# Optimization experiments

Hardware: AMD Instinct MI355X
Metric: run time of the kernel (lower is better)

The kernel has to match this reference:

```python
import jax, jax.numpy as jnp
import numpy as np

B, L, NE, DOUT = 4, 4096, 64, 64
DI = 128          # backbone model dim (hardcoded d_inner in MambaDoc)
NL = 2            # num_layers
H = 2             # num_heads
N = 128           # state_dim
G = 1             # num_groups
CONV = 4          # conv_size
DIN = 2 * DI      # expand=2 -> 256 inner channels of the mixer
P = DIN // H      # headdim = 128
CCH = DIN + 2 * G * N      # 512 conv channels (x, B, C)
DPROJ = 2 * DIN + 2 * G * N + H  # 770 in_proj output width


def setup_inputs() -> dict:
    key = jax.random.key(0)
    ks = jax.random.split(key, 8)
    s = lambda k, shape, sc: (jax.random.normal(k, shape, jnp.float32) * sc)
    return {
        "x": s(ks[0], (B, L, NE), 1.0),
        "in_w": s(ks[1], (DI, NE), (1.0 / NE) ** 0.5),
        "in_b": jnp.zeros((DI,), jnp.float32),
        "out_w": s(ks[2], (DOUT, DI), (1.0 / DI) ** 0.5),
        "out_b": jnp.zeros((DOUT,), jnp.float32),
        "l_rms_w": jnp.ones((NL, DI), jnp.float32),
        "l_in_w": s(ks[3], (NL, DPROJ, DI), (1.0 / DI) ** 0.5),
        "conv_w": s(ks[4], (NL, CCH, CONV), (1.0 / CONV) ** 0.5),
        "conv_b": jnp.zeros((NL, CCH), jnp.float32),
        "dt_bias": s(ks[5], (NL, H), 0.1),
        "A_log": jnp.zeros((NL, H), jnp.float32),   # A = -exp(A_log) = -1
        "D_p": jnp.ones((NL, H), jnp.float32),
        "gnorm_w": jnp.ones((NL, DIN), jnp.float32),
        "l_out_w": s(ks[6], (NL, DI, DIN), (1.0 / DIN) ** 0.5),
        "fnorm_w": jnp.ones((DI,), jnp.float32),
    }


def _rms(x, w, eps=1e-5):
    return x * jax.lax.rsqrt(jnp.mean(x * x, -1, keepdims=True) + eps) * w


def _mamba_layer(x, rms_w, in_w, cw, cb, dtb, a_log, d, gnw, ow):
    # x: (B,L,DI)
    h = _rms(x, rms_w)
    zxbcdt = jnp.einsum("bld,ed->ble", h, in_w)  # (B,L,770)
    z, xBC, dt = jnp.split(zxbcdt, [DIN, DIN + CCH], axis=-1)
    # causal depthwise conv over time, conv_size taps
    xp = jnp.pad(xBC, ((0, 0), (CONV - 1, 0), (0, 0)))
    xc = cb + sum(xp[:, k:k + L, :] * cw[:, k] for k in range(CONV))
    xc = jax.nn.silu(xc)
    xs, Bm, Cm = jnp.split(xc, [DIN, DIN + G * N], axis=-1)
    xs = xs.reshape(B, L, H, P)
    dt = jax.nn.softplus(dt + dtb)                 # (B,L,H)
    dA = jnp.exp(dt * (-jnp.exp(a_log)))           # (B,L,H) discrete decay

    def step(hc, inp):
        dA_t, dt_t, x_t, B_t, C_t = inp  # (B,H),(B,H),(B,H,P),(B,N),(B,N)
        hc = hc * dA_t[:, :, None, None] + (dt_t[:, :, None] * x_t)[..., None] * B_t[:, None, None, :]
        y = jnp.einsum("bhpn,bn->bhp", hc, C_t)
        return hc, y

    h0 = jnp.zeros((B, H, P, N), x.dtype)
    seq = (jnp.moveaxis(dA, 1, 0), jnp.moveaxis(dt, 1, 0), jnp.moveaxis(xs, 1, 0),
           jnp.moveaxis(Bm, 1, 0), jnp.moveaxis(Cm, 1, 0))
    _, ys = jax.lax.scan(step, h0, seq)
    y = jnp.moveaxis(ys, 0, 1)                     # (B,L,H,P)
    y = y + xs * d[None, None, :, None]            # D skip connection
    y = _rms(y.reshape(B, L, DIN) * jax.nn.silu(z), gnw)  # gated RMSNorm
    return x + jnp.einsum("ble,de->bld", y, ow)


def reference(x, in_w, in_b, out_w, out_b, l_rms_w, l_in_w, conv_w, conv_b,
              dt_bias, A_log, D_p, gnorm_w, l_out_w, fnorm_w):
    xp = jnp.einsum("bln,dn->bld", x, in_w) + in_b
    h = xp
    for i in range(NL):
        h = _mamba_layer(h, l_rms_w[i], l_in_w[i], conv_w[i], conv_b[i],
                         dt_bias[i], A_log[i], D_p[i], gnorm_w[i], l_out_w[i])
    h = _rms(h, fnorm_w)            # backbone final norm
    out = xp + h                    # outer residual in MambaDoc.forward
    return jnp.einsum("bld,od->blo", out, out_w) + out_b
```

## Files before the change

### kernel.cpp

```cpp
#include <hip/hip_runtime.h>
#include <cstddef>
#include <cstdint>


#define LSEQ 4096
#define MTOK 16384

typedef unsigned short u16;
typedef _Float16 f16x8 __attribute__((ext_vector_type(8)));
typedef float f32x4 __attribute__((ext_vector_type(4)));

__device__ __forceinline__ u16 f2h(float x) {
    return __builtin_bit_cast(u16, (_Float16)x);
}
__device__ __forceinline__ float h2f(u16 u) {
    return (float)__builtin_bit_cast(_Float16, u);
}
__device__ __forceinline__ float silu_f(float x) { return x / (1.f + __expf(-x)); }

__device__ __forceinline__ void async_lds16(const void* g, void* l) {
    __builtin_amdgcn_global_load_lds(
        (const __attribute__((address_space(1))) unsigned int*)g,
        (__attribute__((address_space(3))) unsigned int*)l, 16, 0, 0);
}

__device__ __forceinline__ uint4 cvt8(const float* __restrict__ src) {
    float4 a = *(const float4*)src;
    float4 b = *(const float4*)(src + 4);
    union { u16 u[8]; uint4 q; } pk;
    pk.u[0] = f2h(a.x); pk.u[1] = f2h(a.y); pk.u[2] = f2h(a.z); pk.u[3] = f2h(a.w);
    pk.u[4] = f2h(b.x); pk.u[5] = f2h(b.y); pk.u[6] = f2h(b.z); pk.u[7] = f2h(b.w);
    return pk.q;
}

__device__ __forceinline__ uint4 cvt8g(const float* __restrict__ src,
                                       const float* __restrict__ gw) {
    float4 a = *(const float4*)src;
    float4 b = *(const float4*)(src + 4);
    float4 ga = *(const float4*)gw;
    float4 gb = *(const float4*)(gw + 4);
    union { u16 u[8]; uint4 q; } pk;
    pk.u[0] = f2h(a.x * ga.x); pk.u[1] = f2h(a.y * ga.y);
    pk.u[2] = f2h(a.z * ga.z); pk.u[3] = f2h(a.w * ga.w);
    pk.u[4] = f2h(b.x * gb.x); pk.u[5] = f2h(b.y * gb.y);
    pk.u[6] = f2h(b.z * gb.z); pk.u[7] = f2h(b.w * gb.w);
    return pk.q;
}

__global__ __launch_bounds__(256) void gemm_rms0_kernel(
    const float* __restrict__ xf, const float* __restrict__ wf,
    const float* __restrict__ bias, const float* __restrict__ rmsw,
    u16* __restrict__ xp16, u16* __restrict__ hbuf16, u16* __restrict__ hn16)
{
    __shared__ u16 sA[64 * 64];
    __shared__ u16 sW[128 * 64];
    __shared__ float red[64][33];
    __shared__ float srstd[64];
    const int m0 = blockIdx.y * 64;
    const int tid = threadIdx.x, wid = tid >> 6, lane = tid & 63;
    const int wm = (wid >> 1) * 32, wn = (wid & 1) * 64;
    const int quad = lane >> 4, cl = lane & 15;
    #pragma unroll
    for (int i = 0; i < 2; i++) {
        int ck = i * 256 + tid;
        int r = ck >> 3, cc = ck & 7;
        int csw = (cc ^ (r & 7)) << 3;
        *(uint4*)&sA[ck * 8] = cvt8(xf + (size_t)(m0 + r) * 64 + csw);
    }
    #pragma unroll
    for (int i = 0; i < 4; i++) {
        int ck = i * 256 + tid;
        int r = ck >> 3, cc = ck & 7;
        int csw = (cc ^ (r & 7)) << 3;
        *(uint4*)&sW[ck * 8] = cvt8(wf + (size_t)r * 64 + csw);
    }
    __syncthreads();
    f32x4 acc[2][4];
    #pragma unroll
    for (int i = 0; i < 2; i++)
        #pragma unroll
        for (int j = 0; j < 4; j++) acc[i][j] = f32x4{0.f, 0.f, 0.f, 0.f};
    #pragma unroll
    for (int ks = 0; ks < 2; ks++) {
        f16x8 af[2], wv[4];
        int kc = ks * 4 + quad;
        #pragma unroll
        for (int i = 0; i < 2; i++) {
            int r = wm + i * 16 + cl;
            af[i] = *(const f16x8*)&sA[r * 64 + ((kc ^ (r & 7)) << 3)];
        }
        #pragma unroll
        for (int j = 0; j < 4; j++) {
            int r = wn + j * 16 + cl;
            wv[j] = *(const f16x8*)&sW[r * 64 + ((kc ^ (r & 7)) << 3)];
        }
        #pragma unroll
        for (int i = 0; i < 2; i++)
            #pragma unroll
            for (int j = 0; j < 4; j++)
                acc[i][j] = __builtin_amdgcn_mfma_f32_16x16x32_f16(
                    af[i], wv[j], acc[i][j], 0, 0, 0);
    }
    const int slot = (wid & 1) * 16 + cl;
    #pragma unroll
    for (int i = 0; i < 2; i++)
        #pragma unroll
        for (int r = 0; r < 4; r++) {
            int t = wm + i * 16 + quad * 4 + r;
            float ssp = 0.f;
            #pragma unroll
            for (int j = 0; j < 4; j++) {
                int n = wn + j * 16 + cl;
                float v = acc[i][j][r] + bias[n];
                acc[i][j][r] = v;
                ssp += v * v;
            }
            red[t][slot] = ssp;
        }
    __syncthreads();
    if (tid < 64) {
        float s = 0.f;
        #pragma unroll
        for (int sl = 0; sl < 32; sl++) s += red[tid][sl];
        srstd[tid] = rsqrtf(s * (1.f / 128.f) + 1e-5f);
    }
    __syncthreads();
    #pragma unroll
    for (int i = 0; i < 2; i++)
        #pragma unroll
        for (int r = 0; r < 4; r++) {
            int t = wm + i * 16 + quad * 4 + r;
            size_t ob = (size_t)(m0 + t) * 128;
            float rstd = srstd[t];
            #pragma unroll
            for (int j = 0; j < 4; j++) {
                int n = wn + j * 16 + cl;
                float v = acc[i][j][r];
                u16 vh = f2h(v);
                xp16[ob + n] = vh;
                hbuf16[ob + n] = vh;
                hn16[ob + n] = f2h(v * rstd * rmsw[n]);
            }
        }
}

__global__ __launch_bounds__(256) void gemm_inproj_kernel(
    const u16* __restrict__ A, const float* __restrict__ Wf,
    u16* __restrict__ zx16, float* __restrict__ dtb, float* __restrict__ Sb,
    const float* __restrict__ dt_bias, const float* __restrict__ A_log)
{
    __shared__ u16 sA[128 * 64];
    __shared__ u16 sW[128 * 64];
    __shared__ float sdt[2][128];
    const int K = 128, N = 770;
    const int n0 = blockIdx.x * 128, m0 = blockIdx.y * 128;
    const int tid = threadIdx.x, wid = tid >> 6, lane = tid & 63;
    const int wm = (wid >> 1) * 64, wn = (wid & 1) * 64;
    const int quad = lane >> 4, cl = lane & 15;
    f32x4 acc[4][4];
    #pragma unroll
    for (int i = 0; i < 4; i++)
        #pragma unroll
        for (int j = 0; j < 4; j++) acc[i][j] = f32x4{0.f, 0.f, 0.f, 0.f};

    for (int k0 = 0; k0 < K; k0 += 64) {
        #pragma unroll
        for (int i = 0; i < 4; i++) {
            int ck = i * 256 + tid;
            int r = ck >> 3, cc = ck & 7;
            int csw = (cc ^ (r & 7)) << 3;
            async_lds16(A + (size_t)(m0 + r) * K + k0 + csw,
                        (void*)(sA + (i * 256 + (tid & ~63)) * 8));
        }
        #pragma unroll
        for (int i = 0; i < 4; i++) {
            int ck = i * 256 + tid;
            int r = ck >> 3, cc = ck & 7;
            int csw = (cc ^ (r & 7)) << 3;
            int rr = n0 + r; if (rr >= N) rr = N - 1;
            *(uint4*)&sW[ck * 8] = cvt8(Wf + (size_t)rr * K + k0 + csw);
        }
        __syncthreads();
        #pragma unroll
        for (int ks = 0; ks < 2; ks++) {
            f16x8 af[4], wv[4];
            int kc = ks * 4 + quad;
            #pragma unroll
            for (int i = 0; i < 4; i++) {
                int r = wm + i * 16 + cl;
                af[i] = *(const f16x8*)&sA[r * 64 + ((kc ^ (r & 7)) << 3)];
            }
            #pragma unroll
            for (int j = 0; j < 4; j++) {
                int r = wn + j * 16 + cl;
                wv[j] = *(const f16x8*)&sW[r * 64 + ((kc ^ (r & 7)) << 3)];
            }
            #pragma unroll
            for (int i = 0; i < 4; i++)
                #pragma unroll
                for (int j = 0; j < 4; j++)
                    acc[i][j] = __builtin_amdgcn_mfma_f32_16x16x32_f16(
                        af[i], wv[j], acc[i][j], 0, 0, 0);
        }
        __syncthreads();
    }
    if (blockIdx.x < 6) {
        #pragma unroll
        for (int i = 0; i < 4; i++) {
            int m = m0 + wm + i * 16 + quad * 4;
            #pragma unroll
            for (int j = 0; j < 4; j++) {
                int n = n0 + wn + j * 16 + cl;
                #pragma unroll
                for (int r = 0; r < 4; r++)
                    zx16[(size_t)(m + r) * 768 + n] = f2h(acc[i][j][r]);
            }
        }
    } else {
        if ((wid & 1) == 0 && cl < 2) {
            #pragma unroll
            for (int i = 0; i < 4; i++)
                #pragma unroll
                for (int r = 0; r < 4; r++)
                    sdt[cl][wm + i * 16 + quad * 4 + r] = acc[i][0][r];
        }
        __syncthreads();
        const int hh = tid >> 7, t = tid & 127;
        float raw = sdt[hh][t] + dt_bias[hh];
        float dt = fmaxf(raw, 0.f) + log1pf(__expf(-fabsf(raw)));
        dtb[(size_t)(m0 + t) * 2 + hh] = dt;
        float ad = -__expf(A_log[hh]) * dt;
        __syncthreads();
        sdt[hh][t] = ad;
        __syncthreads();
        for (int off = 1; off < 128; off <<= 1) {
            float add = (t >= off) ? sdt[hh][t - off] : 0.f;
            __syncthreads();
            sdt[hh][t] += add;
            __syncthreads();
        }
        Sb[(size_t)(m0 + t) * 2 + hh] = sdt[hh][t];
    }
}

__global__ __launch_bounds__(512) void chunkstate_conv_kernel(
    const u16* __restrict__ zx16, const float* __restrict__ cw,
    const float* __restrict__ cb, const float* __restrict__ dtb,
    const float* __restrict__ Sb, u16* __restrict__ Hb)
{
    __shared__ u16 raw[2560 * 8];
    __shared__ u16 XT[128 * 128];
    __shared__ u16 BT[128 * 128];
    __shared__ float scw[2][128][4];
    __shared__ float scb[2][128];
    __shared__ float ssw[128];
    const int c = blockIdx.x, h = blockIdx.y, b = blockIdx.z;
    const int tid = threadIdx.x, wid = tid >> 6, lane = tid & 63;
    const int quad = lane >> 4, cl = lane & 15;
    const int tok0 = b * LSEQ + c * 128;
    for (int idx = tid; idx < 256; idx += 512) {
        int grp = idx >> 7, j = idx & 127;
        int ch = grp ? (256 + j) : (128 * h + j);
        float4 w4 = *(const float4*)&cw[ch * 4];
        scw[grp][j][0] = w4.x; scw[grp][j][1] = w4.y;
        scw[grp][j][2] = w4.z; scw[grp][j][3] = w4.w;
        scb[grp][j] = cb[ch];
    }
    if (tid < 128) {
        float Sl = Sb[(size_t)(tok0 + 127) * 2 + h];
        ssw[tid] = __expf(Sl - Sb[(size_t)(tok0 + tid) * 2 + h])
                   * dtb[(size_t)(tok0 + tid) * 2 + h];
    }
    #pragma unroll
    for (int i = 0; i < 5; i++) {
        int ck = i * 512 + tid;
        int r = ck >> 4; if (r > 130) r = 130;
        int cc = ck & 15;
        int tok = tok0 - 3 + r; if (tok < 0) tok = 0;
        async_lds16(zx16 + (size_t)tok * 768 + 256 + 128 * h + ((cc ^ (r & 15)) << 3),
                    (void*)(raw + (i * 512 + (tid & ~63)) * 8));
    }
    __syncthreads();
    if (c == 0 && tid < 48) *(uint4*)&raw[tid * 8] = make_uint4(0, 0, 0, 0);
    __syncthreads();
    #pragma unroll
    for (int it = 0; it < 4; it++) {
        int idx = it * 512 + tid;
        int s = idx & 127, pg = idx >> 7;
        f16x8 v[4];
        #pragma unroll
        for (int k = 0; k < 4; k++) {
            int rr = s + k;
            v[k] = *(const f16x8*)&raw[rr * 128 + ((pg ^ (rr & 15)) << 3)];
        }
        #pragma unroll
        for (int j = 0; j < 8; j++) {
            int p = pg * 8 + j;
            float o = scb[0][p] + (float)v[0][j] * scw[0][p][0]
                    + (float)v[1][j] * scw[0][p][1]
                    + (float)v[2][j] * scw[0][p][2]
                    + (float)v[3][j] * scw[0][p][3];
            o = silu_f(o);
            XT[p * 128 + (((s >> 3) ^ (p & 15)) << 3) + (s & 7)] = f2h(o);
        }
    }
    __syncthreads();
    #pragma unroll
    for (int i = 0; i < 5; i++) {
        int ck = i * 512 + tid;
        int r = ck >> 4; if (r > 130) r = 130;
        int cc = ck & 15;
        int tok = tok0 - 3 + r; if (tok < 0) tok = 0;
        async_lds16(zx16 + (size_t)tok * 768 + 512 + ((cc ^ (r & 15)) << 3),
                    (void*)(raw + (i * 512 + (tid & ~63)) * 8));
    }
    __syncthreads();
    if (c == 0 && tid < 48) *(uint4*)&raw[tid * 8] = make_uint4(0, 0, 0, 0);
    __syncthreads();
    #pragma unroll
    for (int it = 0; it < 4; it++) {
        int idx = it * 512 + tid;
        int s = idx & 127, ng = idx >> 7;
        f16x8 v[4];
        #pragma unroll
        for (int k = 0; k < 4; k++) {
            int rr = s + k;
            v[k] = *(const f16x8*)&raw[rr * 128 + ((ng ^ (rr & 15)) << 3)];
        }
        float wsv = ssw[s];
        #pragma unroll
        for (int j = 0; j < 8; j++) {
            int n = ng * 8 + j;
            float o = scb[1][n] + (float)v[0][j] * scw[1][n][0]
                    + (float)v[1][j] * scw[1][n][1]
                    + (float)v[2][j] * scw[1][n][2]
                    + (float)v[3][j] * scw[1][n][3];
            o = silu_f(o) * wsv;
            BT[n * 128 + (((s >> 3) ^ (n & 15)) << 3) + (s & 7)] = f2h(o);
        }
    }
    __syncthreads();
    const size_t blk = ((size_t)((b * 2 + h) * 32 + c)) << 14;
    const int wm = (wid >> 1) * 32, wn = (wid & 1) * 64;
    f32x4 acc[2][4];
    #pragma unroll
    for (int i = 0; i < 2; i++)
        #pragma unroll
        for (int j = 0; j < 4; j++) acc[i][j] = f32x4{0.f, 0.f, 0.f, 0.f};
    #pragma unroll
    for (int ks = 0; ks < 4; ks++) {
        f16x8 xa[2], bb[4];
        int kc = ks * 4 + quad;
        #pragma unroll
        for (int i = 0; i < 2; i++) {
            int r = wm + i * 16 + cl;
            xa[i] = *(const f16x8*)&XT[r * 128 + ((kc ^ (r & 15)) << 3)];
        }
        #pragma unroll
        for (int j = 0; j < 4; j++) {
            int r = wn + j * 16 + cl;
            bb[j] = *(const f16x8*)&BT[r * 128 + ((kc ^ (r & 15)) << 3)];
        }
        #pragma unroll
        for (int i = 0; i < 2; i++)
            #pragma unroll
            for (int j = 0; j < 4; j++)
                acc[i][j] = __builtin_amdgcn_mfma_f32_16x16x32_f16(
                    xa[i], bb[j], acc[i][j], 0, 0, 0);
    }
    u16* out = Hb + blk;
    #pragma unroll
    for (int i = 0; i < 2; i++)
        #pragma unroll
        for (int j = 0; j < 4; j++)
            #pragma unroll
            for (int r = 0; r < 4; r++)
                out[(size_t)(wm + i * 16 + quad * 4 + r) * 128 + wn + j * 16 + cl]
                    = f2h(acc[i][j][r]);
}

__global__ __launch_bounds__(256) void statecombine_kernel(
    const float* __restrict__ Sb, const u16* __restrict__ Hb,
    u16* __restrict__ Hbf)
{
    __shared__ float sdec[32];
    const int h = blockIdx.y, b = blockIdx.z;
    const int e2 = blockIdx.x * 256 + threadIdx.x;
    if (threadIdx.x < 32)
        sdec[threadIdx.x] =
            __expf(Sb[(size_t)(b * LSEQ + threadIdx.x * 128 + 127) * 2 + h]);
    const size_t base2 = ((size_t)((b * 2 + h) * 32)) << 13;
    const unsigned int* src = (const unsigned int*)Hb;
    unsigned int* dst = (unsigned int*)Hbf;
    unsigned int v[32];
    #pragma unroll
    for (int c = 0; c < 32; c++)
        v[c] = src[base2 + ((size_t)c << 13) + e2];
    __syncthreads();
    float s0 = 0.f, s1 = 0.f;
    #pragma unroll
    for (int c = 0; c < 32; c++) {
        union { u16 u[2]; unsigned int q; } pk;
        pk.u[0] = f2h(s0); pk.u[1] = f2h(s1);
        dst[base2 + ((size_t)c << 13) + e2] = pk.q;
        float d = sdec[c];
        s0 = d * s0 + h2f((u16)(v[c] & 0xffffu));
        s1 = d * s1 + h2f((u16)(v[c] >> 16));
    }
}

__global__ __launch_bounds__(512) void ssd_ph_kernel(
    const u16* __restrict__ zx16, const u16* __restrict__ Hbf,
    const float* __restrict__ dtb, const float* __restrict__ Sb,
    const float* __restrict__ cw, const float* __restrict__ cb,
    const float* __restrict__ Dp, u16* __restrict__ g16)
{
    __shared__ u16 raw[2560 * 8];
    __shared__ u16 XT[128 * 128];
    __shared__ u16 Btok[128 * 128];
    __shared__ u16 Ctok[128 * 128];
    __shared__ float sS[128], sdt[128];
    __shared__ float scw[3][128][4];
    __shared__ float scb[3][128];
    const int c = blockIdx.x, h = blockIdx.y, b = blockIdx.z;
    const int tid = threadIdx.x, wid = tid >> 6, lane = tid & 63;
    const int quad = lane >> 4, cl = lane & 15;
    const int tok0 = b * LSEQ + c * 128;
    const size_t blk = ((size_t)((b * 2 + h) * 32 + c)) << 14;
    for (int idx = tid; idx < 384; idx += 512) {
        int grp = idx >> 7, j = idx & 127;
        int ch = (grp == 0) ? (128 * h + j) : (grp == 1 ? 256 + j : 384 + j);
        float4 w4 = *(const float4*)&cw[ch * 4];
        scw[grp][j][0] = w4.x; scw[grp][j][1] = w4.y;
        scw[grp][j][2] = w4.z; scw[grp][j][3] = w4.w;
        scb[grp][j] = cb[ch];
    }
    if (tid < 128) {
        sS[tid] = Sb[(size_t)(tok0 + tid) * 2 + h];
        sdt[tid] = dtb[(size_t)(tok0 + tid) * 2 + h];
    }
    #pragma unroll
    for (int i = 0; i < 5; i++) {
        int ck = i * 512 + tid;
        int r = ck >> 4; if (r > 130) r = 130;
        int cc = ck & 15;
        int tok = tok0 - 3 + r; if (tok < 0) tok = 0;
        async_lds16(zx16 + (size_t)tok * 768 + 256 + 128 * h + ((cc ^ (r & 15)) << 3),
                    (void*)(raw + (i * 512 + (tid & ~63)) * 8));
    }
    __syncthreads();
    if (c == 0 && tid < 48) *(uint4*)&raw[tid * 8] = make_uint4(0, 0, 0, 0);
    __syncthreads();
    #pragma unroll
    for (int it = 0; it < 4; it++) {
        int idx = it * 512 + tid;
        int s = idx & 127, pg = idx >> 7;
        f16x8 v[4];
        #pragma unroll
        for (int k = 0; k < 4; k++) {
            int rr = s + k;
            v[k] = *(const f16x8*)&raw[rr * 128 + ((pg ^ (rr & 15)) << 3)];
        }
        #pragma unroll
        for (int j = 0; j < 8; j++) {
            int p = pg * 8 + j;
            float o = scb[0][p] + (float)v[0][j] * scw[0][p][0]
                    + (float)v[1][j] * scw[0][p][1]
                    + (float)v[2][j] * scw[0][p][2]
                    + (float)v[3][j] * scw[0][p][3];
            XT[p * 128 + (((s >> 3) ^ (p & 15)) << 3) + (s & 7)] = f2h(silu_f(o));
        }
    }
    __syncthreads();
    #pragma unroll
    for (int i = 0; i < 5; i++) {
        int ck = i * 512 + tid;
        int r = ck >> 4; if (r > 130) r = 130;
        int cc = ck & 15;
        int tok = tok0 - 3 + r; if (tok < 0) tok = 0;
        async_lds16(zx16 + (size_t)tok * 768 + 512 + ((cc ^ (r & 15)) << 3),
                    (void*)(raw + (i * 512 + (tid & ~63)) * 8));
    }
    __syncthreads();
    if (c == 0 && tid < 48) *(uint4*)&raw[tid * 8] = make_uint4(0, 0, 0, 0);
    __syncthreads();
    #pragma unroll
    for (int it = 0; it < 4; it++) {
        int idx = it * 512 + tid;
        int t = idx & 127, ng = idx >> 7;
        f16x8 v[4];
        #pragma unroll
        for (int k = 0; k < 4; k++) {
            int rr = t + k;
            v[k] = *(const f16x8*)&raw[rr * 128 + ((ng ^ (rr & 15)) << 3)];
        }
        union { u16 u[8]; uint4 q; } pk;
        #pragma unroll
        for (int j = 0; j < 8; j++) {
            int n = ng * 8 + j;
            float o = scb[1][n] + (float)v[0][j] * scw[1][n][0]
                    + (float)v[1][j] * scw[1][n][1]
                    + (float)v[2][j] * scw[1][n][2]
                    + (float)v[3][j] * scw[1][n][3];
            pk.u[j] = f2h(silu_f(o));
        }
        *(uint4*)&Btok[t * 128 + ((ng ^ (t & 15)) << 3)] = pk.q;
    }
    __syncthreads();
    #pragma unroll
    for (int i = 0; i < 5; i++) {
        int ck = i * 512 + tid;
        int r = ck >> 4; if (r > 130) r = 130;
        int cc = ck & 15;
        int tok = tok0 - 3 + r; if (tok < 0) tok = 0;
        async_lds16(zx16 + (size_t)tok * 768 + 640 + ((cc ^ (r & 15)) << 3),
                    (void*)(raw + (i * 512 + (tid & ~63)) * 8));
    }
    __syncthreads();
    if (c == 0 && tid < 48) *(uint4*)&raw[tid * 8] = make_uint4(0, 0, 0, 0);
    __syncthreads();
    #pragma unroll
    for (int it = 0; it < 4; it++) {
        int idx = it * 512 + tid;
        int t = idx & 127, ng = idx >> 7;
        f16x8 v[4];
        #pragma unroll
        for (int k = 0; k < 4; k++) {
            int rr = t + k;
            v[k] = *(const f16x8*)&raw[rr * 128 + ((ng ^ (rr & 15)) << 3)];
        }
        union { u16 u[8]; uint4 q; } pk;
        #pragma unroll
        for (int j = 0; j < 8; j++) {
            int n = ng * 8 + j;
            float o = scb[2][n] + (float)v[0][j] * scw[2][n][0]
                    + (float)v[1][j] * scw[2][n][1]
                    + (float)v[2][j] * scw[2][n][2]
                    + (float)v[3][j] * scw[2][n][3];
            pk.u[j] = f2h(silu_f(o));
        }
        *(uint4*)&Ctok[t * 128 + ((ng ^ (t & 15)) << 3)] = pk.q;
    }
    __syncthreads();
    #pragma unroll
    for (int i = 0; i < 4; i++) {
        int ck = i * 512 + tid;
        int r = ck >> 4, cc = ck & 15;
        async_lds16(Hbf + blk + (size_t)r * 128 + ((cc ^ (r & 15)) << 3),
                    (void*)(raw + (i * 512 + (tid & ~63)) * 8));
    }
    __syncthreads();
    const int wm = (wid >> 1) * 32, wn = (wid & 1) * 64;
    f32x4 acc[2][4];
    #pragma unroll
    for (int i = 0; i < 2; i++)
        #pragma unroll
        for (int j = 0; j < 4; j++) acc[i][j] = f32x4{0.f, 0.f, 0.f, 0.f};
    #pragma unroll
    for (int ks = 0; ks < 4; ks++) {
        f16x8 ca[2], hb[4];
        int kc = ks * 4 + quad;
        #pragma unroll
        for (int i = 0; i < 2; i++) {
            int r = wm + i * 16 + cl;
            ca[i] = *(const f16x8*)&Ctok[r * 128 + ((kc ^ (r & 15)) << 3)];
        }
        #pragma unroll
        for (int j = 0; j < 4; j++) {
            int r = wn + j * 16 + cl;
            hb[j] = *(const f16x8*)&raw[r * 128 + ((kc ^ (r & 15)) << 3)];
        }
        #pragma unroll
        for (int i = 0; i < 2; i++)
            #pragma unroll
            for (int j = 0; j < 4; j++)
                acc[i][j] = __builtin_amdgcn_mfma_f32_16x16x32_f16(
                    ca[i], hb[j], acc[i][j], 0, 0, 0);
    }
    #pragma unroll
    for (int i = 0; i < 2; i++)
        #pragma unroll
        for (int r = 0; r < 4; r++) {
            float e = __expf(sS[wm + i * 16 + quad * 4 + r]);
            #pragma unroll
            for (int j = 0; j < 4; j++) acc[i][j][r] *= e;
        }
    f32x4 sacc[2][4];
    #pragma unroll
    for (int i = 0; i < 2; i++)
        #pragma unroll
        for (int j = 0; j < 4; j++) sacc[i][j] = f32x4{0.f, 0.f, 0.f, 0.f};
    #pragma unroll
    for (int ks = 0; ks < 4; ks++) {
        f16x8 cs[2], bs[4];
        int kc = ks * 4 + quad;
        #pragma unroll
        for (int i2 = 0; i2 < 2; i2++) {
            int r = wm + i2 * 16 + cl;
            cs[i2] = *(const f16x8*)&Ctok[r * 128 + ((kc ^ (r & 15)) << 3)];
        }
        #pragma unroll
        for (int j = 0; j < 4; j++) {
            int r = wn + j * 16 + cl;
            bs[j] = *(const f16x8*)&Btok[r * 128 + ((kc ^ (r & 15)) << 3)];
        }
        #pragma unroll
        for (int i2 = 0; i2 < 2; i2++)
            #pragma unroll
            for (int j = 0; j < 4; j++)
                if (wm + i2 * 16 + 15 >= wn + j * 16)
                    sacc[i2][j] = __builtin_amdgcn_mfma_f32_16x16x32_f16(
                        cs[i2], bs[j], sacc[i2][j], 0, 0, 0);
    }
    __syncthreads();
    #pragma unroll
    for (int i2 = 0; i2 < 2; i2++)
        #pragma unroll
        for (int r = 0; r < 4; r++) {
            int t = wm + i2 * 16 + quad * 4 + r;
            float Stv = sS[t];
            #pragma unroll
            for (int j = 0; j < 4; j++) {
                int s = wn + j * 16 + cl;
                float gv = 0.f;
                if (s <= t) gv = sacc[i2][j][r] * __expf(Stv - sS[s]) * sdt[s];
                raw[t * 128 + (((s >> 3) ^ (t & 15)) << 3) + (s & 7)] = f2h(gv);
            }
        }
    __syncthreads();
    #pragma unroll
    for (int ks = 0; ks < 4; ks++) {
        f16x8 ga[2], xb[4];
        int kc = ks * 4 + quad;
        #pragma unroll
        for (int i = 0; i < 2; i++) {
            int r = wm + i * 16 + cl;
            ga[i] = *(const f16x8*)&raw[r * 128 + ((kc ^ (r & 15)) << 3)];
        }
        #pragma unroll
        for (int j = 0; j < 4; j++) {
            int r = wn + j * 16 + cl;
            xb[j] = *(const f16x8*)&XT[r * 128 + ((kc ^ (r & 15)) << 3)];
        }
        #pragma unroll
        for (int i = 0; i < 2; i++)
            #pragma unroll
            for (int j = 0; j < 4; j++)
                acc[i][j] = __builtin_amdgcn_mfma_f32_16x16x32_f16(
                    ga[i], xb[j], acc[i][j], 0, 0, 0);
    }
    const float dco = Dp[h];
    #pragma unroll
    for (int i = 0; i < 2; i++)
        #pragma unroll
        for (int r = 0; r < 4; r++) {
            int t = wm + i * 16 + quad * 4 + r;
            u16* row = g16 + (size_t)(tok0 + t) * 256 + h * 128;
            #pragma unroll
            for (int j = 0; j < 4; j++) {
                int p = wn + j * 16 + cl;
                float xv = h2f(XT[p * 128 + (((t >> 3) ^ (p & 15)) << 3) + (t & 7)]);
                float zv = h2f(zx16[(size_t)(tok0 + t) * 768 + h * 128 + p]);
                row[p] = f2h((acc[i][j][r] + dco * xv) * silu_f(zv));
            }
        }
}

__global__ __launch_bounds__(256) void gemm_outrms_kernel(
    const u16* __restrict__ A, const float* __restrict__ Wf,
    const float* __restrict__ gnw, const float* __restrict__ rmsw,
    u16* __restrict__ xp16, u16* __restrict__ hbuf16, u16* __restrict__ hn16,
    const float* __restrict__ out_wf, const float* __restrict__ out_b,
    float* __restrict__ dout, int mode)
{
    __shared__ u16 sA[64 * 64];
    __shared__ u16 sW[128 * 64];
    __shared__ float red[64][33];
    __shared__ float srstd[64];
    __shared__ float redp[64][5];
    __shared__ float rstdg[64];
    __shared__ u16 hn2[64 * 128];
    __shared__ u16 ow[64 * 128];
    const int K = 256;
    const int m0 = blockIdx.y * 64;
    const int tid = threadIdx.x, wid = tid >> 6, lane = tid & 63;
    const int wm = (wid >> 1) * 32, wn = (wid & 1) * 64;
    const int quad = lane >> 4, cl = lane & 15;
    {
        int t = tid >> 2, q = tid & 3;
        const u16* row = A + (size_t)(m0 + t) * 256 + q * 64;
        float ss = 0.f;
        #pragma unroll
        for (int u = 0; u < 8; u++) {
            f16x8 v = *(const f16x8*)&row[u * 8];
            #pragma unroll
            for (int j = 0; j < 8; j++) { float f = (float)v[j]; ss += f * f; }
        }
        redp[t][q] = ss;
    }
    __syncthreads();
    if (tid < 64)
        rstdg[tid] = rsqrtf((redp[tid][0] + redp[tid][1] + redp[tid][2]
                             + redp[tid][3]) * (1.f / 256.f) + 1e-5f);
    f32x4 acc[2][4];
    #pragma unroll
    for (int i = 0; i < 2; i++)
        #pragma unroll
        for (int j = 0; j < 4; j++) acc[i][j] = f32x4{0.f, 0.f, 0.f, 0.f};

    for (int k0 = 0; k0 < K; k0 += 64) {
        #pragma unroll
        for (int i = 0; i < 2; i++) {
            int ck = i * 256 + tid;
            int r = ck >> 3, cc = ck & 7;
            int csw = (cc ^ (r & 7)) << 3;
            async_lds16(A + (size_t)(m0 + r) * K + k0 + csw,
                        (void*)(sA + (i * 256 + (tid & ~63)) * 8));
        }
        #pragma unroll
        for (int i = 0; i < 4; i++) {
            int ck = i * 256 + tid;
            int r = ck >> 3, cc = ck & 7;
            int csw = (cc ^ (r & 7)) << 3;
            *(uint4*)&sW[ck * 8] = cvt8g(Wf + (size_t)r * K + k0 + csw,
                                         gnw + k0 + csw);
        }
        __syncthreads();
        #pragma unroll
        for (int ks = 0; ks < 2; ks++) {
            f16x8 af[2], wv[4];
            int kc = ks * 4 + quad;
            #pragma unroll
            for (int i = 0; i < 2; i++) {
                int r = wm + i * 16 + cl;
                af[i] = *(const f16x8*)&sA[r * 64 + ((kc ^ (r & 7)) << 3)];
            }
            #pragma unroll
            for (int j = 0; j < 4; j++) {
                int r = wn + j * 16 + cl;
                wv[j] = *(const f16x8*)&sW[r * 64 + ((kc ^ (r & 7)) << 3)];
            }
            #pragma unroll
            for (int i = 0; i < 2; i++)
                #pragma unroll
                for (int j = 0; j < 4; j++)
                    acc[i][j] = __builtin_amdgcn_mfma_f32_16x16x32_f16(
                        af[i], wv[j], acc[i][j], 0, 0, 0);
        }
        __syncthreads();
    }
    const int slot = (wid & 1) * 16 + cl;
    #pragma unroll
    for (int i = 0; i < 2; i++)
        #pragma unroll
        for (int r = 0; r < 4; r++) {
            int t = wm + i * 16 + quad * 4 + r;
            size_t ob = (size_t)(m0 + t) * 128;
            float rg = rstdg[t];
            float ssp = 0.f;
            #pragma unroll
            for (int j = 0; j < 4; j++) {
                int n = wn + j * 16 + cl;
                float v = acc[i][j][r] * rg + h2f(hbuf16[ob + n]);
                acc[i][j][r] = v;
                ssp += v * v;
            }
            red[t][slot] = ssp;
        }
    __syncthreads();
    if (tid < 64) {
        float s = 0.f;
        #pragma unroll
        for (int sl = 0; sl < 32; sl++) s += red[tid][sl];
        srstd[tid] = rsqrtf(s * (1.f / 128.f) + 1e-5f);
    }
    __syncthreads();
    #pragma unroll
    for (int i = 0; i < 2; i++)
        #pragma unroll
        for (int r = 0; r < 4; r++) {
            int t = wm + i * 16 + quad * 4 + r;
            size_t ob = (size_t)(m0 + t) * 128;
            float rstd = srstd[t];
            #pragma unroll
            for (int j = 0; j < 4; j++) {
                int n = wn + j * 16 + cl;
                float v = acc[i][j][r];
                float val = v * rstd * rmsw[n];
                if (mode == 1) {
                    hbuf16[ob + n] = f2h(v);
                    hn16[ob + n] = f2h(val);
                } else {
                    val += h2f(xp16[ob + n]);
                    hn2[t * 128 + (((n >> 3) ^ (t & 15)) << 3) + (n & 7)] = f2h(val);
                }
            }
        }
    if (mode == 1) return;
    #pragma unroll
    for (int i = 0; i < 4; i++) {
        int ck = i * 256 + tid;
        int rr = ck >> 4, cc = ck & 15;
        int csw = (cc ^ (rr & 15)) << 3;
        *(uint4*)&ow[ck * 8] = cvt8(out_wf + (size_t)rr * 128 + csw);
    }
    __syncthreads();
    const int wm4 = (wid >> 1) * 32, wn4 = (wid & 1) * 32;
    f32x4 acc2[2][2];
    #pragma unroll
    for (int i = 0; i < 2; i++)
        #pragma unroll
        for (int j = 0; j < 2; j++) acc2[i][j] = f32x4{0.f, 0.f, 0.f, 0.f};
    #pragma unroll
    for (int ks = 0; ks < 4; ks++) {
        f16x8 af2[2], wf2[2];
        int kc = ks * 4 + quad;
        #pragma unroll
        for (int i = 0; i < 2; i++) {
            int r = wm4 + i * 16 + cl;
            af2[i] = *(const f16x8*)&hn2[r * 128 + ((kc ^ (r & 15)) << 3)];
        }
        #pragma unroll
        for (int j = 0; j < 2; j++) {
            int rr = wn4 + j * 16 + cl;
            wf2[j] = *(const f16x8*)&ow[rr * 128 + ((kc ^ (rr & 15)) << 3)];
        }
        #pragma unroll
        for (int i = 0; i < 2; i++)
            #pragma unroll
            for (int j = 0; j < 2; j++)
                acc2[i][j] = __builtin_amdgcn_mfma_f32_16x16x32_f16(
                    af2[i], wf2[j], acc2[i][j], 0, 0, 0);
    }
    #pragma unroll
    for (int i = 0; i < 2; i++) {
        int m = m0 + wm4 + i * 16 + quad * 4;
        #pragma unroll
        for (int j = 0; j < 2; j++) {
            int n = wn4 + j * 16 + cl;
            float bv = out_b[n];
            #pragma unroll
            for (int r = 0; r < 4; r++)
                dout[(size_t)(m + r) * 64 + n] = acc2[i][j][r] + bv;
        }
    }
}

extern "C" void kernel_launch(void* const* d_in, const int* in_sizes, int n_in,
                              void* d_out, int out_size, void* d_ws, size_t ws_size,
                              hipStream_t stream)
{
    (void)in_sizes; (void)n_in; (void)out_size; (void)ws_size;
    const float* x       = (const float*)d_in[0];
    const float* in_w    = (const float*)d_in[1];
    const float* in_b    = (const float*)d_in[2];
    const float* out_w   = (const float*)d_in[3];
    const float* out_b   = (const float*)d_in[4];
    const float* l_rms_w = (const float*)d_in[5];
    const float* l_in_w  = (const float*)d_in[6];
    const float* conv_w  = (const float*)d_in[7];
    const float* conv_b  = (const float*)d_in[8];
    const float* dt_bias = (const float*)d_in[9];
    const float* A_log   = (const float*)d_in[10];
    const float* D_p     = (const float*)d_in[11];
    const float* gnorm_w = (const float*)d_in[12];
    const float* l_out_w = (const float*)d_in[13];
    const float* fnorm_w = (const float*)d_in[14];

    char* w = (char*)d_ws;
    u16*   xp16   = (u16*)(w);
    u16*   hbuf16 = (u16*)(w + 4194304);
    u16*   hn16   = (u16*)(w + 8388608);
    u16*   zx16   = (u16*)(w + 12582912);
    float* dtb    = (float*)(w + 37748736);
    float* Sb     = (float*)(w + 37879808);
    u16*   Hb     = (u16*)(w + 38010880);
    u16*   Hbf    = (u16*)(w + 46399488);
    u16*   g16    = (u16*)(w + 54788096);

    gemm_rms0_kernel<<<dim3(1, 256), 256, 0, stream>>>(
        x, in_w, in_b, l_rms_w, xp16, hbuf16, hn16);

    for (int i = 0; i < 2; i++) {
        gemm_inproj_kernel<<<dim3(7, 128), 256, 0, stream>>>(
            hn16, l_in_w + (size_t)i * 770 * 128, zx16, dtb, Sb,
            dt_bias + i * 2, A_log + i * 2);
        chunkstate_conv_kernel<<<dim3(32, 2, 4), 512, 0, stream>>>(
            zx16, conv_w + i * 2048, conv_b + i * 512, dtb, Sb, Hb);
        statecombine_kernel<<<dim3(32, 2, 4), 256, 0, stream>>>(Sb, Hb, Hbf);
        ssd_ph_kernel<<<dim3(32, 2, 4), 512, 0, stream>>>(
            zx16, Hbf, dtb, Sb, conv_w + i * 2048, conv_b + i * 512,
            D_p + i * 2, g16);
        gemm_outrms_kernel<<<dim3(1, 256), 256, 0, stream>>>(
            g16, l_out_w + (size_t)i * 128 * 256, gnorm_w + i * 256,
            (i == 0) ? (l_rms_w + 128) : fnorm_w, xp16, hbuf16, hn16,
            out_w, out_b, (float*)d_out, (i == 0) ? 1 : 3);
    }
}
```

Before: 226.9 us.

## Fold dt projection into last in_proj tile, preload Hbf to registers, fuse RMS sums

The in_proj GEMM grid drops its seventh column of blocks, which computed only two useful dt columns. Block column 5 now also computes those two dot products with scalar FMAs and then runs the softplus and prefix scan. The SSD kernel loads the chunk state straight from global memory into registers at kernel start instead of staging it through LDS, which removes a barrier. The out-projection kernel accumulates the gated RMS sum of squares from the A tiles already staged in LDS rather than making a separate pass over global memory. The trade-offs are extra serial work in block column 5 and higher register pressure in the SSD kernel.

```diff
diff --git a/kernel.cpp b/kernel.cpp
--- a/kernel.cpp
+++ b/kernel.cpp
@@ -152,7 +152,7 @@
     __shared__ u16 sA[128 * 64];
     __shared__ u16 sW[128 * 64];
     __shared__ float sdt[2][128];
-    const int K = 128, N = 770;
+    const int K = 128;
     const int n0 = blockIdx.x * 128, m0 = blockIdx.y * 128;
     const int tid = threadIdx.x, wid = tid >> 6, lane = tid & 63;
     const int wm = (wid >> 1) * 64, wn = (wid & 1) * 64;
@@ -177,8 +177,7 @@
             int ck = i * 256 + tid;
             int r = ck >> 3, cc = ck & 7;
             int csw = (cc ^ (r & 7)) << 3;
-            int rr = n0 + r; if (rr >= N) rr = N - 1;
-            *(uint4*)&sW[ck * 8] = cvt8(Wf + (size_t)rr * K + k0 + csw);
+            *(uint4*)&sW[ck * 8] = cvt8(Wf + (size_t)(n0 + r) * K + k0 + csw);
         }
         __syncthreads();
         #pragma unroll
@@ -204,30 +203,30 @@
         }
         __syncthreads();
     }
-    if (blockIdx.x < 6) {
-        #pragma unroll
-        for (int i = 0; i < 4; i++) {
-            int m = m0 + wm + i * 16 + quad * 4;
-            #pragma unroll
-            for (int j = 0; j < 4; j++) {
-                int n = n0 + wn + j * 16 + cl;
-                #pragma unroll
-                for (int r = 0; r < 4; r++)
-                    zx16[(size_t)(m + r) * 768 + n] = f2h(acc[i][j][r]);
-            }
-        }
-    } else {
-        if ((wid & 1) == 0 && cl < 2) {
-            #pragma unroll
-            for (int i = 0; i < 4; i++)
-                #pragma unroll
-                for (int r = 0; r < 4; r++)
-                    sdt[cl][wm + i * 16 + quad * 4 + r] = acc[i][0][r];
-        }
-        __syncthreads();
-        const int hh = tid >> 7, t = tid & 127;
-        float raw = sdt[hh][t] + dt_bias[hh];
-        float dt = fmaxf(raw, 0.f) + log1pf(__expf(-fabsf(raw)));
+    #pragma unroll
+    for (int i = 0; i < 4; i++) {
+        int m = m0 + wm + i * 16 + quad * 4;
+        #pragma unroll
+        for (int j = 0; j < 4; j++) {
+            int n = n0 + wn + j * 16 + cl;
+            #pragma unroll
+            for (int r = 0; r < 4; r++)
+                zx16[(size_t)(m + r) * 768 + n] = f2h(acc[i][j][r]);
+        }
+    }
+    if (blockIdx.x == 5) {
+        const int t = tid >> 1, hh = tid & 1;
+        const u16* arow = A + (size_t)(m0 + t) * 128;
+        const float* wrow = Wf + (size_t)(768 + hh) * 128;
+        float dot = 0.f;
+        #pragma unroll
+        for (int k = 0; k < 128; k += 8) {
+            f16x8 av = *(const f16x8*)&arow[k];
+            #pragma unroll
+            for (int j = 0; j < 8; j++) dot += (float)av[j] * wrow[k + j];
+        }
+        float rawv = dot + dt_bias[hh];
+        float dt = fmaxf(rawv, 0.f) + log1pf(__expf(-fabsf(rawv)));
         dtb[(size_t)(m0 + t) * 2 + hh] = dt;
         float ad = -__expf(A_log[hh]) * dt;
         __syncthreads();
@@ -427,6 +426,16 @@
     const int quad = lane >> 4, cl = lane & 15;
     const int tok0 = b * LSEQ + c * 128;
     const size_t blk = ((size_t)((b * 2 + h) * 32 + c)) << 14;
+    const int wm = (wid >> 1) * 32, wn = (wid & 1) * 64;
+    f16x8 hinreg[4][4];
+    #pragma unroll
+    for (int ks = 0; ks < 4; ks++)
+        #pragma unroll
+        for (int j = 0; j < 4; j++) {
+            int r = wn + j * 16 + cl;
+            int kc = ks * 4 + quad;
+            hinreg[ks][j] = *(const f16x8*)&Hbf[blk + (size_t)r * 128 + kc * 8];
+        }
     for (int idx = tid; idx < 384; idx += 512) {
         int grp = idx >> 7, j = idx & 127;
         int ch = (grp == 0) ? (128 * h + j) : (grp == 1 ? 256 + j : 384 + j);
@@ -542,15 +551,6 @@
         *(uint4*)&Ctok[t * 128 + ((ng ^ (t & 15)) << 3)] = pk.q;
     }
     __syncthreads();
-    #pragma unroll
-    for (int i = 0; i < 4; i++) {
-        int ck = i * 512 + tid;
-        int r = ck >> 4, cc = ck & 15;
-        async_lds16(Hbf + blk + (size_t)r * 128 + ((cc ^ (r & 15)) << 3),
-                    (void*)(raw + (i * 512 + (tid & ~63)) * 8));
-    }
-    __syncthreads();
-    const int wm = (wid >> 1) * 32, wn = (wid & 1) * 64;
     f32x4 acc[2][4];
     #pragma unroll
     for (int i = 0; i < 2; i++)
@@ -558,7 +558,7 @@
         for (int j = 0; j < 4; j++) acc[i][j] = f32x4{0.f, 0.f, 0.f, 0.f};
     #pragma unroll
     for (int ks = 0; ks < 4; ks++) {
-        f16x8 ca[2], hb[4];
+        f16x8 ca[2];
         int kc = ks * 4 + quad;
         #pragma unroll
         for (int i = 0; i < 2; i++) {
@@ -566,16 +566,11 @@
             ca[i] = *(const f16x8*)&Ctok[r * 128 + ((kc ^ (r & 15)) << 3)];
         }
         #pragma unroll
-        for (int j = 0; j < 4; j++) {
-            int r = wn + j * 16 + cl;
-            hb[j] = *(const f16x8*)&raw[r * 128 + ((kc ^ (r & 15)) << 3)];
-        }
-        #pragma unroll
         for (int i = 0; i < 2; i++)
             #pragma unroll
             for (int j = 0; j < 4; j++)
                 acc[i][j] = __builtin_amdgcn_mfma_f32_16x16x32_f16(
-                    ca[i], hb[j], acc[i][j], 0, 0, 0);
+                    ca[i], hinreg[ks][j], acc[i][j], 0, 0, 0);
     }
     #pragma unroll
     for (int i = 0; i < 2; i++)
@@ -612,7 +607,6 @@
                     sacc[i2][j] = __builtin_amdgcn_mfma_f32_16x16x32_f16(
                         cs[i2], bs[j], sacc[i2][j], 0, 0, 0);
     }
-    __syncthreads();
     #pragma unroll
     for (int i2 = 0; i2 < 2; i2++)
         #pragma unroll
@@ -686,28 +680,13 @@
     const int tid = threadIdx.x, wid = tid >> 6, lane = tid & 63;
     const int wm = (wid >> 1) * 32, wn = (wid & 1) * 64;
     const int quad = lane >> 4, cl = lane & 15;
-    {
-        int t = tid >> 2, q = tid & 3;
-        const u16* row = A + (size_t)(m0 + t) * 256 + q * 64;
-        float ss = 0.f;
-        #pragma unroll
-        for (int u = 0; u < 8; u++) {
-            f16x8 v = *(const f16x8*)&row[u * 8];
-            #pragma unroll
-            for (int j = 0; j < 8; j++) { float f = (float)v[j]; ss += f * f; }
-        }
-        redp[t][q] = ss;
-    }
-    __syncthreads();
-    if (tid < 64)
-        rstdg[tid] = rsqrtf((redp[tid][0] + redp[tid][1] + redp[tid][2]
-                             + redp[tid][3]) * (1.f / 256.f) + 1e-5f);
     f32x4 acc[2][4];
     #pragma unroll
     for (int i = 0; i < 2; i++)
         #pragma unroll
         for (int j = 0; j < 4; j++) acc[i][j] = f32x4{0.f, 0.f, 0.f, 0.f};
 
+    float ssq = 0.f;
     for (int k0 = 0; k0 < K; k0 += 64) {
         #pragma unroll
         for (int i = 0; i < 2; i++) {
@@ -726,6 +705,16 @@
                                          gnw + k0 + csw);
         }
         __syncthreads();
+        {
+            int rr = tid >> 2, q = tid & 3;
+            f16x8 v0 = *(const f16x8*)&sA[rr * 64 + q * 16];
+            f16x8 v1 = *(const f16x8*)&sA[rr * 64 + q * 16 + 8];
+            #pragma unroll
+            for (int j = 0; j < 8; j++) {
+                float a = (float)v0[j], bq = (float)v1[j];
+                ssq += a * a + bq * bq;
+            }
+        }
         #pragma unroll
         for (int ks = 0; ks < 2; ks++) {
             f16x8 af[2], wv[4];
@@ -749,6 +738,12 @@
         }
         __syncthreads();
     }
+    redp[tid >> 2][tid & 3] = ssq;
+    __syncthreads();
+    if (tid < 64)
+        rstdg[tid] = rsqrtf((redp[tid][0] + redp[tid][1] + redp[tid][2]
+                             + redp[tid][3]) * (1.f / 256.f) + 1e-5f);
+    __syncthreads();
     const int slot = (wid & 1) * 16 + cl;
     #pragma unroll
     for (int i = 0; i < 2; i++)
@@ -882,7 +877,7 @@
         x, in_w, in_b, l_rms_w, xp16, hbuf16, hn16);
 
     for (int i = 0; i < 2; i++) {
-        gemm_inproj_kernel<<<dim3(7, 128), 256, 0, stream>>>(
+        gemm_inproj_kernel<<<dim3(6, 128), 256, 0, stream>>>(
             hn16, l_in_w + (size_t)i * 770 * 128, zx16, dtb, Sb,
             dt_bias + i * 2, A_log + i * 2);
         chunkstate_conv_kernel<<<dim3(32, 2, 4), 512, 0, stream>>>(
```

Result: slower. 243.5 us (+7.3%).
